# Kernel optimization log

Hardware: AMD Instinct MI355X
Metric: run time of the kernel (lower is better)

The kernel has to match this reference:

```python
import jax, jax.numpy as jnp
import numpy as np

SIZES = [4096, 12288, 20480, 20480, 8192]  # atoms of degree 0..4 (atoms sorted by degree)
N_ATOMS = sum(SIZES)
BATCH = 1024
N_TASKS, N_CLASSES = 12, 2
BN_EPS = 1e-3  # keras BatchNormalization default epsilon


def setup_inputs() -> dict:
    key = jax.random.key(0)
    ks = jax.random.split(key, 20)
    inp = {}
    inp["atom_features"] = jax.random.normal(ks[0], (N_ATOMS, 75), jnp.float32)
    starts = np.concatenate([[0], np.cumsum(SIZES)[:-1]])
    inp["degree_slice"] = jnp.asarray(np.stack([starts, np.array(SIZES)], 1), jnp.int32)
    inp["membership"] = jax.random.randint(ks[1], (N_ATOMS,), 0, BATCH, jnp.int32)
    inp["n_samples"] = BATCH
    for d in range(1, 5):
        inp[f"deg_adj_{d}"] = jax.random.randint(ks[1 + d], (SIZES[d], d), 0, N_ATOMS, jnp.int32)

    def w(k, shape, s=0.05):
        return s * jax.random.normal(k, shape, jnp.float32)

    # GraphConv weights: order [relW_deg1, selfW_deg1, ..., relW_deg4, selfW_deg4, selfW_deg0]
    inp["gc1_W"] = w(ks[6], (9, 75, 256)); inp["gc1_b"] = w(ks[7], (9, 256))
    inp["gc2_W"] = w(ks[8], (9, 256, 256)); inp["gc2_b"] = w(ks[9], (9, 256))

    def bn_params(k, c):  # rows: gamma, beta, moving_mean, moving_var
        g = 1.0 + 0.1 * jax.random.normal(k, (c,), jnp.float32)
        b = 0.1 * jax.random.normal(jax.random.fold_in(k, 1), (c,), jnp.float32)
        return jnp.stack([g, b, jnp.zeros((c,), jnp.float32), jnp.ones((c,), jnp.float32)])

    inp["bn1"] = bn_params(ks[10], 256)
    inp["bn2"] = bn_params(ks[11], 256)
    inp["bn3"] = bn_params(ks[12], 512)
    inp["dense_W"] = w(ks[13], (256, 512)); inp["dense_b"] = w(ks[14], (512,))
    inp["head_W"] = w(ks[15], (2 * 512, N_TASKS * N_CLASSES)); inp["head_b"] = w(ks[16], (N_TASKS * N_CLASSES,))
    return inp


def _graph_conv(x, adjs, W, b):
    # degree-0 atoms: self transform only (last weight matrix)
    pieces = [x[: SIZES[0]] @ W[8] + b[8]]
    off = SIZES[0]
    for d in range(1, 5):
        nd = SIZES[d]
        self_atoms = x[off: off + nd]
        rel = jnp.take(x, adjs[d - 1], axis=0).sum(axis=1)  # [nd, F] neighbor sum
        out = rel @ W[2 * (d - 1)] + b[2 * (d - 1)] + self_atoms @ W[2 * d - 1] + b[2 * d - 1]
        pieces.append(out)
        off += nd
    return jax.nn.relu(jnp.concatenate(pieces, axis=0))


def _graph_pool(x, adjs):
    pieces = [x[: SIZES[0]]]  # degree-0: passthrough
    off = SIZES[0]
    for d in range(1, 5):
        nd = SIZES[d]
        self_atoms = x[off: off + nd]
        neigh = jnp.take(x, adjs[d - 1], axis=0)  # [nd, d, F]
        pieces.append(jnp.maximum(self_atoms, neigh.max(axis=1)))
        off += nd
    return jnp.concatenate(pieces, axis=0)


def _bn(x, p):  # inference batchnorm with moving stats
    g, b, m, v = p
    return g * (x - m) * jax.lax.rsqrt(v + BN_EPS) + b


def reference(atom_features, degree_slice, membership, n_samples,
              deg_adj_1, deg_adj_2, deg_adj_3, deg_adj_4,
              gc1_W, gc1_b, gc2_W, gc2_b, bn1, bn2, bn3,
              dense_W, dense_b, head_W, head_b):
    adjs = (deg_adj_1, deg_adj_2, deg_adj_3, deg_adj_4)
    x = atom_features
    for W, b, bn in ((gc1_W, gc1_b, bn1), (gc2_W, gc2_b, bn2)):
        x = _bn(_graph_conv(x, adjs, W, b), bn)
        x = _graph_pool(x, adjs)
    h = _bn(jax.nn.relu(x @ dense_W + dense_b), bn3)  # [N_ATOMS, 512]
    # GraphGather: per-molecule sum and max, tanh activation
    seg_sum = jax.ops.segment_sum(h, membership, num_segments=BATCH)
    seg_max = jax.ops.segment_max(h, membership, num_segments=BATCH)
    fp = jnp.tanh(jnp.concatenate([seg_sum, seg_max], axis=1))  # neural fingerprint [BATCH, 1024]
    logits = (fp @ head_W + head_b).reshape(BATCH, N_TASKS, N_CLASSES)[: int(n_samples)]  # trim
    return jax.nn.softmax(logits, axis=-1), logits, fp
```

## Files before the change

kernel.cpp:

```cpp
#include <hip/hip_runtime.h>
#include <hip/hip_bf16.h>
#include <math.h>

#define NA 65536
#define MAXSEG 160

typedef _Float16 half8 __attribute__((ext_vector_type(8)));
typedef _Float16 h4    __attribute__((ext_vector_type(4)));
typedef float float4v  __attribute__((ext_vector_type(4)));

typedef __attribute__((address_space(3))) unsigned int lds_uint;
typedef __attribute__((address_space(1))) const unsigned int g_uint;

__device__ __forceinline__ void async16(const void* g, void* l) {
    __builtin_amdgcn_global_load_lds((g_uint*)g, (lds_uint*)l, 16, 0, 0);
}


__device__ __forceinline__ int unperm128(int p) {
    return (p & ~127) + (((p & 127) & 7) << 4) + ((p & 127) >> 3);
}

__device__ __forceinline__ unsigned mapf(float x) {
    unsigned b = __float_as_uint(x);
    return (b & 0x80000000u) ? ~b : (b | 0x80000000u);
}
#define MAPF_NEGINF 0x007FFFFFu

__device__ __forceinline__ void atom_seg(int atom, int& d, int& loc,
                                         const int* a1, const int* a2,
                                         const int* a3, const int* a4,
                                         const int*& adj) {
    if (atom < 4096)       { d = 0; loc = 0; adj = nullptr; }
    else if (atom < 16384) { d = 1; adj = a1; loc = atom - 4096; }
    else if (atom < 36864) { d = 2; adj = a2; loc = atom - 16384; }
    else if (atom < 57344) { d = 3; adj = a3; loc = atom - 36864; }
    else                   { d = 4; adj = a4; loc = atom - 57344; }
}

__global__ __launch_bounds__(256) void prep_kernel(
    const float* __restrict__ af,
    const float* __restrict__ gc1W, const float* __restrict__ gc1b,
    const float* __restrict__ gc2W, const float* __restrict__ gc2b,
    const float* __restrict__ dW, const float* __restrict__ hW,
    _Float16* __restrict__ af16, _Float16* __restrict__ Wc1, float* __restrict__ bias1,
    _Float16* __restrict__ Wc2, float* __restrict__ bias2,
    _Float16* __restrict__ dWt, float* __restrict__ hWt, int* __restrict__ count) {
    int b = blockIdx.x, t = threadIdx.x;
    if (b < 5120) {
        int idx = b * 256 + t;
        int atom = idx / 20, k4 = idx - atom * 20;
        int c0 = k4 * 4;
        h4 o;
        #pragma unroll
        for (int j = 0; j < 4; j++) {
            int c = c0 + j;
            o[j] = (_Float16)((c < 75) ? af[(size_t)atom * 75 + c] : 0.f);
        }
        *(h4*)(af16 + (size_t)atom * 80 + c0) = o;
    } else if (b < 5920) {
        int idx = (b - 5120) * 256 + t;
        if (idx < 204800) {
            int k = idx % 160, n = (idx / 160) & 255, seg = idx / (160 * 256);
            float v = 0.f;
            if (k < 80) {
                if (k < 75) { int w = (seg == 0) ? 8 : (2 * seg - 1); v = gc1W[(w * 75 + k) * 256 + n]; }
            } else {
                int kk = k - 80;
                if (kk < 75 && seg > 0) { int w = 2 * (seg - 1); v = gc1W[(w * 75 + kk) * 256 + n]; }
            }
            Wc1[(size_t)(seg * 256 + n) * 160 + k] = (_Float16)v;
        }
        if (idx < 1280) {
            int n = idx & 255, seg = idx >> 8;
            bias1[idx] = (seg == 0) ? gc1b[8 * 256 + n]
                                    : gc1b[(2 * seg - 1) * 256 + n] + gc1b[2 * (seg - 1) * 256 + n];
        }
    } else if (b < 8480) {
        int idx = (b - 5920) * 256 + t;
        int k = idx & 511, n = (idx >> 9) & 255, seg = idx >> 17;
        float v = 0.f;
        if (k < 256) {
            int w = (seg == 0) ? 8 : (2 * seg - 1);
            v = gc2W[(w * 256 + unperm128(k)) * 256 + n];
        } else if (seg > 0) {
            int w = 2 * (seg - 1);
            v = gc2W[(w * 256 + unperm128(k - 256)) * 256 + n];
        }
        Wc2[(size_t)(seg * 256 + n) * 512 + k] = (_Float16)v;
        if (idx < 1280) {
            int nn = idx & 255, sg = idx >> 8;
            bias2[idx] = (sg == 0) ? gc2b[8 * 256 + nn]
                                   : gc2b[(2 * sg - 1) * 256 + nn] + gc2b[2 * (sg - 1) * 256 + nn];
        }
    } else if (b < 8992) {
        int idx = (b - 8480) * 256 + t;
        int n = idx >> 8, k = idx & 255;
        dWt[(size_t)n * 256 + k] = (_Float16)dW[(size_t)unperm128(k) * 512 + n];
    } else if (b < 9088) {
        int idx = (b - 8992) * 256 + t;
        int o = idx / 1024, k = idx & 1023;
        hWt[idx] = hW[k * 24 + o];
    } else {
        int i = (b - 9088) * 256 + t;
        if (i < 1024) count[i] = 0;
    }
}

__global__ void bucket_kernel(const int* __restrict__ mem, int* __restrict__ count,
                              int* __restrict__ list) {
    int i = blockIdx.x * 256 + threadIdx.x;
    int seg = mem[i];
    int pos = atomicAdd(&count[seg], 1);
    if (pos < MAXSEG) list[seg * MAXSEG + pos] = i;
}

__global__ __launch_bounds__(1024) void scan_kernel(const int* __restrict__ count,
                                                    int* __restrict__ offs) {
    __shared__ int tmp[1024];
    int t = threadIdx.x;
    int v = count[t]; if (v > MAXSEG) v = MAXSEG;
    tmp[t] = v;
    __syncthreads();
    for (int off = 1; off < 1024; off <<= 1) {
        int x = (t >= off) ? tmp[t - off] : 0;
        __syncthreads();
        tmp[t] += x;
        __syncthreads();
    }
    offs[t] = tmp[t] - v;
}

__global__ __launch_bounds__(256) void build_sorted_kernel(
    const int* __restrict__ count, const int* __restrict__ offs,
    const int* __restrict__ list, int* __restrict__ sorted, int* __restrict__ ipos) {
    int seg = blockIdx.x;
    int n = count[seg]; if (n > MAXSEG) n = MAXSEG;
    int base = offs[seg];
    for (int i = threadIdx.x; i < n; i += 256) {
        int atom = list[seg * MAXSEG + i];
        sorted[base + i] = atom | (seg << 16);
        ipos[atom] = base + i;
    }
}

__global__ __launch_bounds__(256) void gather1n_kernel(
    const _Float16* __restrict__ af16,
    const int* __restrict__ a1, const int* __restrict__ a2,
    const int* __restrict__ a3, const int* __restrict__ a4,
    _Float16* __restrict__ Xn1) {
    int idx = blockIdx.x * 256 + threadIdx.x;
    int atom = idx / 20, k4 = idx - atom * 20;
    int c0 = k4 * 4;
    int d, loc; const int* adj;
    atom_seg(atom, d, loc, a1, a2, a3, a4, adj);
    float s0 = 0.f, s1 = 0.f, s2 = 0.f, s3 = 0.f;
    for (int j = 0; j < d; j++) {
        int nb = adj[(size_t)loc * d + j];
        h4 v = *(const h4*)(af16 + (size_t)nb * 80 + c0);
        s0 += (float)v[0]; s1 += (float)v[1]; s2 += (float)v[2]; s3 += (float)v[3];
    }
    h4 o; o[0] = (_Float16)s0; o[1] = (_Float16)s1; o[2] = (_Float16)s2; o[3] = (_Float16)s3;
    *(h4*)(Xn1 + (size_t)atom * 80 + c0) = o;
}

__global__ __launch_bounds__(256) void gather2n_kernel(
    const _Float16* __restrict__ p,
    const int* __restrict__ a1, const int* __restrict__ a2,
    const int* __restrict__ a3, const int* __restrict__ a4,
    _Float16* __restrict__ Xn) {
    int atom = blockIdx.x * 8 + (threadIdx.x >> 5);
    int l = threadIdx.x & 31;
    int d, loc; const int* adj;
    atom_seg(atom, d, loc, a1, a2, a3, a4, adj);
    float s[8] = {};
    for (int j = 0; j < d; j++) {
        int nb = adj[(size_t)loc * d + j];
        half8 v = *(const half8*)(p + (size_t)nb * 256 + l * 8);
        #pragma unroll
        for (int e = 0; e < 8; e++) s[e] += (float)v[e];
    }
    half8 o;
    #pragma unroll
    for (int e = 0; e < 8; e++) o[e] = (_Float16)s[e];
    *(half8*)(Xn + (size_t)atom * 256 + l * 8) = o;
}

template<int K, int N, int BK, int SB>
__global__ __launch_bounds__(256) void gemm_kernel(
    const _Float16* __restrict__ X, const _Float16* __restrict__ Xn,
    const _Float16* __restrict__ Wt,
    const float* __restrict__ bias, const float* __restrict__ bnp,
    int wstride, int bstride, _Float16* __restrict__ out) {
    constexpr int NC8 = BK / 8;
    constexpr int MASK = NC8 - 1;
    __shared__ __align__(16) _Float16 As[128 * BK];
    __shared__ __align__(16) _Float16 Bs[128 * BK];
    constexpr int nb = N / 128;
    int G = gridDim.x;
    int bid = (blockIdx.x & 7) * (G >> 3) + (blockIdx.x >> 3);
    int m0 = (bid / nb) * 128, n0 = (bid % nb) * 128;
    int t = m0 >> 7;
    int seg = (t < 32) ? 0 : (t < 128) ? 1 : (t < 288) ? 2 : (t < 448) ? 3 : 4;
    const _Float16* Wb = Wt + (size_t)seg * wstride;
    const float* bia = bias + seg * bstride;
    int tid = threadIdx.x, lane = tid & 63, wave = tid >> 6;
    int wm = (wave >> 1) * 64, wn = (wave & 1) * 64;
    int lrow = lane & 15, lq = lane >> 4;
    float4v acc[4][4] = {};
    for (int kc = 0; kc < K / BK; kc++) {
        #pragma unroll
        for (int q = 0; q < NC8 / 2; q++) {
            int slot = q * 256 + wave * 64 + lane;
            int row = slot / NC8;
            int cs = slot & MASK;
            int c8 = cs ^ (row & MASK);
            const _Float16* gA;
            if (SB == 0) {
                gA = X + (size_t)(m0 + row) * K + kc * BK + c8 * 8;
            } else {
                int kcol = kc * BK + c8 * 8;
                gA = (kcol < SB) ? X  + (size_t)(m0 + row) * SB + kcol
                                 : Xn + (size_t)(m0 + row) * SB + (kcol - SB);
            }
            async16(gA, As + (size_t)(q * 256 + wave * 64) * 8);
            const _Float16* gB = Wb + (size_t)(n0 + row) * K + kc * BK + c8 * 8;
            async16(gB, Bs + (size_t)(q * 256 + wave * 64) * 8);
        }
        __syncthreads();
        #pragma unroll
        for (int kl = 0; kl < BK / 32; kl++) {
            half8 af[4], bf[4];
            #pragma unroll
            for (int i = 0; i < 4; i++) {
                int ra = wm + i * 16 + lrow;
                int ca = (kl * 4 + lq) ^ (ra & MASK);
                af[i] = *(const half8*)(As + ra * BK + ca * 8);
                int rb = wn + i * 16 + lrow;
                int cb = (kl * 4 + lq) ^ (rb & MASK);
                bf[i] = *(const half8*)(Bs + rb * BK + cb * 8);
            }
            #pragma unroll
            for (int mi = 0; mi < 4; mi++)
                #pragma unroll
                for (int ni = 0; ni < 4; ni++)
                    acc[mi][ni] = __builtin_amdgcn_mfma_f32_16x16x32_f16(af[mi], bf[ni], acc[mi][ni], 0, 0, 0);
        }
        __syncthreads();
    }
    float bv[4], sc[4], mn[4], be[4];
    #pragma unroll
    for (int ni = 0; ni < 4; ni++) {
        int c = n0 + wn + ni * 16 + lrow;
        bv[ni] = bia[c];
        float g = bnp[c], vr = bnp[3 * N + c];
        mn[ni] = bnp[2 * N + c]; be[ni] = bnp[N + c];
        sc[ni] = g * rsqrtf(vr + 1e-3f);
    }
    int p0 = n0 + lrow * 8 + (wave & 1) * 4;
    #pragma unroll
    for (int mi = 0; mi < 4; mi++) {
        #pragma unroll
        for (int r = 0; r < 4; r++) {
            h4 pack;
            #pragma unroll
            for (int ni = 0; ni < 4; ni++) {
                float v = acc[mi][ni][r] + bv[ni];
                v = fmaxf(v, 0.f);
                v = sc[ni] * (v - mn[ni]) + be[ni];
                pack[ni] = (_Float16)v;
            }
            int row = m0 + wm + mi * 16 + lq * 4 + r;
            *(h4*)(out + (size_t)row * N + p0) = pack;
        }
    }
}

__global__ __launch_bounds__(256) void pool_f16_kernel(
    const _Float16* __restrict__ x,
    const int* __restrict__ a1, const int* __restrict__ a2,
    const int* __restrict__ a3, const int* __restrict__ a4,
    const int* __restrict__ remap,
    _Float16* __restrict__ out) {
    int atom = blockIdx.x * 8 + (threadIdx.x >> 5);
    int l = threadIdx.x & 31;
    int d, loc; const int* adj;
    atom_seg(atom, d, loc, a1, a2, a3, a4, adj);
    half8 m = *(const half8*)(x + (size_t)atom * 256 + l * 8);
    float mv[8];
    #pragma unroll
    for (int e = 0; e < 8; e++) mv[e] = (float)m[e];
    for (int j = 0; j < d; j++) {
        int nb = adj[(size_t)loc * d + j];
        half8 v = *(const half8*)(x + (size_t)nb * 256 + l * 8);
        #pragma unroll
        for (int e = 0; e < 8; e++) mv[e] = fmaxf(mv[e], (float)v[e]);
    }
    half8 o;
    #pragma unroll
    for (int e = 0; e < 8; e++) o[e] = (_Float16)mv[e];
    int orow = remap ? remap[atom] : atom;
    *(half8*)(out + (size_t)orow * 256 + l * 8) = o;
}

__global__ __launch_bounds__(256) void dense_kernel(
    const _Float16* __restrict__ X, const _Float16* __restrict__ Wt,
    const float* __restrict__ bias, const float* __restrict__ bnp,
    const int* __restrict__ sorted,
    float* __restrict__ psum, unsigned* __restrict__ pmax) {
    constexpr int NBINS = 4;
    __shared__ __align__(16) _Float16 As[64 * 64];
    __shared__ __align__(16) _Float16 Bs[128 * 64];
    __shared__ float binsum[NBINS * 128];
    __shared__ unsigned binmax[NBINS * 128];
    __shared__ int spk[64];
    int G = gridDim.x;
    int bid = (blockIdx.x & 7) * (G >> 3) + (blockIdx.x >> 3);
    int m0 = (bid >> 2) * 64, n0 = (bid & 3) * 128;
    int tid = threadIdx.x, lane = tid & 63, wave = tid >> 6;
    if (tid < 64) spk[tid] = sorted[m0 + tid];
    for (int e = tid; e < NBINS * 128; e += 256) { binsum[e] = 0.f; binmax[e] = MAPF_NEGINF; }
    __syncthreads();
    int wm = (wave & 1) * 32, wn = (wave >> 1) * 64;
    int lrow = lane & 15, lq = lane >> 4;
    float4v acc[2][4] = {};
    for (int kc = 0; kc < 4; kc++) {
        #pragma unroll
        for (int q = 0; q < 2; q++) {
            int slot = q * 256 + wave * 64 + lane;
            int row = slot >> 3, cs = slot & 7, c8 = cs ^ (row & 7);
            async16(X + (size_t)(m0 + row) * 256 + kc * 64 + c8 * 8,
                    As + (size_t)(q * 256 + wave * 64) * 8);
        }
        #pragma unroll
        for (int q = 0; q < 4; q++) {
            int slot = q * 256 + wave * 64 + lane;
            int row = slot >> 3, cs = slot & 7, c8 = cs ^ (row & 7);
            async16(Wt + (size_t)(n0 + row) * 256 + kc * 64 + c8 * 8,
                    Bs + (size_t)(q * 256 + wave * 64) * 8);
        }
        __syncthreads();
        #pragma unroll
        for (int kl = 0; kl < 2; kl++) {
            half8 af[2], bf[4];
            #pragma unroll
            for (int i = 0; i < 2; i++) {
                int ra = wm + i * 16 + lrow;
                int ca = (kl * 4 + lq) ^ (ra & 7);
                af[i] = *(const half8*)(As + ra * 64 + ca * 8);
            }
            #pragma unroll
            for (int j = 0; j < 4; j++) {
                int rb = wn + j * 16 + lrow;
                int cb = (kl * 4 + lq) ^ (rb & 7);
                bf[j] = *(const half8*)(Bs + rb * 64 + cb * 8);
            }
            #pragma unroll
            for (int mi = 0; mi < 2; mi++)
                #pragma unroll
                for (int ni = 0; ni < 4; ni++)
                    acc[mi][ni] = __builtin_amdgcn_mfma_f32_16x16x32_f16(af[mi], bf[ni], acc[mi][ni], 0, 0, 0);
        }
        __syncthreads();
    }
    float bv[4], sc[4], mn[4], be[4];
    #pragma unroll
    for (int ni = 0; ni < 4; ni++) {
        int c = n0 + wn + ni * 16 + lrow;
        bv[ni] = bias[c];
        float g = bnp[c], vr = bnp[3 * 512 + c];
        mn[ni] = bnp[2 * 512 + c]; be[ni] = bnp[512 + c];
        sc[ni] = g * rsqrtf(vr + 1e-3f);
    }
    int pcol = lrow * 8 + (wave >> 1) * 4;
    int segbase = spk[0] >> 16;
    #pragma unroll
    for (int mi = 0; mi < 2; mi++) {
        int r0 = wm + mi * 16;
        int sFirst = spk[r0] >> 16, sLast = spk[r0 + 15] >> 16;
        if (sFirst == sLast) {
            int srel = sFirst - segbase; if (srel > NBINS - 1) srel = NBINS - 1;
            float ps[4], pm[4];
            #pragma unroll
            for (int ni = 0; ni < 4; ni++) { ps[ni] = 0.f; pm[ni] = -INFINITY; }
            #pragma unroll
            for (int r = 0; r < 4; r++) {
                #pragma unroll
                for (int ni = 0; ni < 4; ni++) {
                    float v = acc[mi][ni][r] + bv[ni];
                    v = fmaxf(v, 0.f);
                    v = sc[ni] * (v - mn[ni]) + be[ni];
                    ps[ni] += v;
                    pm[ni] = fmaxf(pm[ni], v);
                }
            }
            #pragma unroll
            for (int ni = 0; ni < 4; ni++) {
                ps[ni] += __shfl_xor(ps[ni], 16, 64);
                ps[ni] += __shfl_xor(ps[ni], 32, 64);
                pm[ni] = fmaxf(pm[ni], __shfl_xor(pm[ni], 16, 64));
                pm[ni] = fmaxf(pm[ni], __shfl_xor(pm[ni], 32, 64));
            }
            if (lq == 0) {
                int bb = srel * 128 + pcol;
                #pragma unroll
                for (int ni = 0; ni < 4; ni++) {
                    atomicAdd(&binsum[bb + ni], ps[ni]);
                    atomicMax(&binmax[bb + ni], mapf(pm[ni]));
                }
            }
        } else {
            int curs = -1;
            float ps[4], pm[4];
            #pragma unroll
            for (int r = 0; r < 4; r++) {
                int row = r0 + lq * 4 + r;
                int srel = (spk[row] >> 16) - segbase;
                if (srel > NBINS - 1) srel = NBINS - 1;
                if (srel != curs) {
                    if (curs >= 0) {
                        int bb = curs * 128 + pcol;
                        #pragma unroll
                        for (int ni = 0; ni < 4; ni++) {
                            atomicAdd(&binsum[bb + ni], ps[ni]);
                            atomicMax(&binmax[bb + ni], mapf(pm[ni]));
                        }
                    }
                    curs = srel;
                    #pragma unroll
                    for (int ni = 0; ni < 4; ni++) { ps[ni] = 0.f; pm[ni] = -INFINITY; }
                }
                #pragma unroll
                for (int ni = 0; ni < 4; ni++) {
                    float v = acc[mi][ni][r] + bv[ni];
                    v = fmaxf(v, 0.f);
                    v = sc[ni] * (v - mn[ni]) + be[ni];
                    ps[ni] += v;
                    pm[ni] = fmaxf(pm[ni], v);
                }
            }
            {
                int bb = curs * 128 + pcol;
                #pragma unroll
                for (int ni = 0; ni < 4; ni++) {
                    atomicAdd(&binsum[bb + ni], ps[ni]);
                    atomicMax(&binmax[bb + ni], mapf(pm[ni]));
                }
            }
        }
    }
    __syncthreads();
    int nseg = (spk[63] >> 16) - segbase + 1;
    if (nseg > NBINS) nseg = NBINS;
    int tile = m0 >> 6;
    for (int e = tid; e < nseg * 128; e += 256) {
        int s = e >> 7, pc = e & 127;
        size_t slot = ((size_t)(tile * NBINS + s)) * 512 + n0 + pc;
        psum[slot] = binsum[e];
        pmax[slot] = binmax[e];
    }
}

__global__ __launch_bounds__(256) void head_kernel(
    const float* __restrict__ psum, const unsigned* __restrict__ pmax,
    const int* __restrict__ count, const int* __restrict__ offs,
    const int* __restrict__ sorted,
    const float* __restrict__ hWt, const float* __restrict__ hb,
    float* __restrict__ fp, float* __restrict__ logits, float* __restrict__ probs) {
    constexpr int NBINS = 4;
    __shared__ float fps[1024];
    __shared__ float red[32];
    int s = blockIdx.x;
    int t = threadIdx.x;
    int cnt = count[s]; if (cnt > MAXSEG) cnt = MAXSEG;
    int off = offs[s];
    float sum0 = 0.f, sum1 = 0.f;
    unsigned mu0 = MAPF_NEGINF, mu1 = MAPF_NEGINF;
    if (cnt > 0) {
        int t0 = off >> 6, t1 = (off + cnt - 1) >> 6;
        for (int tt = t0; tt <= t1; tt++) {
            int segbase_t = sorted[tt << 6] >> 16;
            int srel = s - segbase_t;
            if (srel < 0) srel = 0;
            if (srel > NBINS - 1) srel = NBINS - 1;
            const float* ps = psum + ((size_t)(tt * NBINS + srel)) * 512;
            const unsigned* pm = pmax + ((size_t)(tt * NBINS + srel)) * 512;
            sum0 += ps[t]; sum1 += ps[t + 256];
            unsigned a0 = pm[t], a1 = pm[t + 256];
            mu0 = (a0 > mu0) ? a0 : mu0;
            mu1 = (a1 > mu1) ? a1 : mu1;
        }
    }
    {
        float sv = tanhf(sum0);
        unsigned b = (mu0 & 0x80000000u) ? (mu0 & 0x7FFFFFFFu) : ~mu0;
        float mv = tanhf(__uint_as_float(b));
        int chan = unperm128(t);
        fps[chan] = sv; fps[512 + chan] = mv;
        fp[(size_t)s * 1024 + chan] = sv;
        fp[(size_t)s * 1024 + 512 + chan] = mv;
    }
    {
        float sv = tanhf(sum1);
        unsigned b = (mu1 & 0x80000000u) ? (mu1 & 0x7FFFFFFFu) : ~mu1;
        float mv = tanhf(__uint_as_float(b));
        int chan = unperm128(t + 256);
        fps[chan] = sv; fps[512 + chan] = mv;
        fp[(size_t)s * 1024 + chan] = sv;
        fp[(size_t)s * 1024 + 512 + chan] = mv;
    }
    __syncthreads();
    int o = t >> 3, kp = t & 7;
    float acc = 0.f;
    if (o < 24) {
        const float* w = hWt + (size_t)o * 1024 + kp * 128;
        const float* f = fps + kp * 128;
        #pragma unroll 8
        for (int i = 0; i < 128; i++) acc = fmaf(f[i], w[i], acc);
    }
    acc += __shfl_down(acc, 4, 64);
    acc += __shfl_down(acc, 2, 64);
    acc += __shfl_down(acc, 1, 64);
    if (o < 24 && kp == 0) red[o] = acc + hb[o];
    __syncthreads();
    if (t < 24) {
        float a = red[t];
        float an = red[t ^ 1];
        logits[(size_t)s * 24 + t] = a;
        probs[(size_t)s * 24 + t] = 1.f / (1.f + expf(an - a));
    }
}

extern "C" void kernel_launch(void* const* d_in, const int* in_sizes, int n_in,
                              void* d_out, int out_size, void* d_ws, size_t ws_size,
                              hipStream_t stream) {
    const float* af         = (const float*)d_in[0];
    const int*   membership = (const int*)d_in[2];
    const int*   a1 = (const int*)d_in[4];
    const int*   a2 = (const int*)d_in[5];
    const int*   a3 = (const int*)d_in[6];
    const int*   a4 = (const int*)d_in[7];
    const float* gc1W = (const float*)d_in[8];
    const float* gc1b = (const float*)d_in[9];
    const float* gc2W = (const float*)d_in[10];
    const float* gc2b = (const float*)d_in[11];
    const float* bn1  = (const float*)d_in[12];
    const float* bn2  = (const float*)d_in[13];
    const float* bn3  = (const float*)d_in[14];
    const float* dW   = (const float*)d_in[15];
    const float* db   = (const float*)d_in[16];
    const float* hW   = (const float*)d_in[17];
    const float* hb   = (const float*)d_in[18];

    float* out    = (float*)d_out;
    float* probs  = out;
    float* logits = out + 24576;
    float* fp     = out + 49152;

    _Float16* Wc1  = (_Float16*)d_ws;
    _Float16* Wc2  = Wc1 + 204800;
    _Float16* dWt  = Wc2 + 655360;
    float* bias1   = (float*)(dWt + 131072);
    float* bias2   = bias1 + 1280;
    float* hWt     = bias2 + 1280;
    float* psum    = hWt + 24576;
    unsigned* pmax = (unsigned*)(psum + 2097152);
    int* count     = (int*)(pmax + 2097152);
    int* offs      = count + 1024;
    int* sorted    = offs + 1024;
    int* ipos      = sorted + 65536;
    int* list      = ipos + 65536;
    _Float16* bufSm  = (_Float16*)(list + 163840);
    _Float16* Xn     = bufSm + (size_t)NA * 160;
    _Float16* bufY   = Xn + (size_t)NA * 256;
    _Float16* bufP   = bufY + (size_t)NA * 256;
    _Float16* af16 = bufSm;
    _Float16* Xn1  = bufSm + (size_t)NA * 80;

    prep_kernel<<<9092, 256, 0, stream>>>(af, gc1W, gc1b, gc2W, gc2b, dW, hW,
                                          af16, Wc1, bias1, Wc2, bias2, dWt, hWt, count);
    bucket_kernel<<<256, 256, 0, stream>>>(membership, count, list);
    scan_kernel<<<1, 1024, 0, stream>>>(count, offs);
    build_sorted_kernel<<<1024, 256, 0, stream>>>(count, offs, list, sorted, ipos);
    gather1n_kernel<<<5120, 256, 0, stream>>>(af16, a1, a2, a3, a4, Xn1);
    gemm_kernel<160, 256, 32, 80><<<1024, 256, 0, stream>>>(af16, Xn1, Wc1, bias1, bn1,
                                                            256 * 160, 256, bufY);
    pool_f16_kernel<<<8192, 256, 0, stream>>>(bufY, a1, a2, a3, a4, nullptr, bufP);
    gather2n_kernel<<<8192, 256, 0, stream>>>(bufP, a1, a2, a3, a4, Xn);
    gemm_kernel<512, 256, 64, 256><<<1024, 256, 0, stream>>>(bufP, Xn, Wc2, bias2, bn2,
                                                             256 * 512, 256, bufY);
    pool_f16_kernel<<<8192, 256, 0, stream>>>(bufY, a1, a2, a3, a4, ipos, bufP);
    dense_kernel<<<4096, 256, 0, stream>>>(bufP, dWt, db, bn3, sorted, psum, pmax);
    head_kernel<<<1024, 256, 0, stream>>>(psum, pmax, count, offs, sorted,
                                          hWt, hb, fp, logits, probs);
}
```

Before: 308.3 us.

## Keep dense weight tile resident in LDS and double-buffer 256-row activation tiles

The dense+BN+gather kernel now gives each block four 64-row subtiles (256 rows). It loads the full-K 128x256 weight slab into LDS once and double-buffers the activation subtiles, prefetching the next while computing the current one. This cuts repeated weight reloads and per-k-chunk barriers, and the grid shrinks from 4096 to 1024 blocks. The per-tile segment bins double to 8, and the head kernel now indexes 256-row tiles. The cost is about 136KB of LDS per block, which limits occupancy to one block per CU. There is also a small risk of bin clamping if a 256-row tile spans more than 8 molecules.

```diff
diff --git a/kernel.cpp b/kernel.cpp
--- a/kernel.cpp
+++ b/kernel.cpp
@@ -308,61 +308,38 @@
     const float* __restrict__ bias, const float* __restrict__ bnp,
     const int* __restrict__ sorted,
     float* __restrict__ psum, unsigned* __restrict__ pmax) {
-    constexpr int NBINS = 4;
-    __shared__ __align__(16) _Float16 As[64 * 64];
-    __shared__ __align__(16) _Float16 Bs[128 * 64];
+    constexpr int NBINS = 8;
+    __shared__ __align__(16) _Float16 Bs[128 * 256];
+    __shared__ __align__(16) _Float16 As[2][64 * 256];
     __shared__ float binsum[NBINS * 128];
     __shared__ unsigned binmax[NBINS * 128];
-    __shared__ int spk[64];
+    __shared__ int spk[256];
     int G = gridDim.x;
     int bid = (blockIdx.x & 7) * (G >> 3) + (blockIdx.x >> 3);
-    int m0 = (bid >> 2) * 64, n0 = (bid & 3) * 128;
+    int mg = bid >> 2, n0 = (bid & 3) * 128;
+    int m_base = mg * 256;
     int tid = threadIdx.x, lane = tid & 63, wave = tid >> 6;
-    if (tid < 64) spk[tid] = sorted[m0 + tid];
+    spk[tid] = sorted[m_base + tid];
     for (int e = tid; e < NBINS * 128; e += 256) { binsum[e] = 0.f; binmax[e] = MAPF_NEGINF; }
+    #pragma unroll
+    for (int q = 0; q < 16; q++) {
+        int slot = q * 256 + wave * 64 + lane;
+        int row = slot >> 5, c32 = slot & 31, kcg = c32 >> 3, cs = c32 & 7;
+        int c8 = cs ^ (row & 7);
+        async16(Wt + (size_t)(n0 + row) * 256 + kcg * 64 + c8 * 8,
+                Bs + (size_t)slot * 8);
+    }
+    #pragma unroll
+    for (int q = 0; q < 8; q++) {
+        int slot = q * 256 + wave * 64 + lane;
+        int row = slot >> 5, c32 = slot & 31, kcg = c32 >> 3, cs = c32 & 7;
+        int c8 = cs ^ (row & 7);
+        async16(X + (size_t)(m_base + row) * 256 + kcg * 64 + c8 * 8,
+                As[0] + (size_t)slot * 8);
+    }
     __syncthreads();
     int wm = (wave & 1) * 32, wn = (wave >> 1) * 64;
     int lrow = lane & 15, lq = lane >> 4;
-    float4v acc[2][4] = {};
-    for (int kc = 0; kc < 4; kc++) {
-        #pragma unroll
-        for (int q = 0; q < 2; q++) {
-            int slot = q * 256 + wave * 64 + lane;
-            int row = slot >> 3, cs = slot & 7, c8 = cs ^ (row & 7);
-            async16(X + (size_t)(m0 + row) * 256 + kc * 64 + c8 * 8,
-                    As + (size_t)(q * 256 + wave * 64) * 8);
-        }
-        #pragma unroll
-        for (int q = 0; q < 4; q++) {
-            int slot = q * 256 + wave * 64 + lane;
-            int row = slot >> 3, cs = slot & 7, c8 = cs ^ (row & 7);
-            async16(Wt + (size_t)(n0 + row) * 256 + kc * 64 + c8 * 8,
-                    Bs + (size_t)(q * 256 + wave * 64) * 8);
-        }
-        __syncthreads();
-        #pragma unroll
-        for (int kl = 0; kl < 2; kl++) {
-            half8 af[2], bf[4];
-            #pragma unroll
-            for (int i = 0; i < 2; i++) {
-                int ra = wm + i * 16 + lrow;
-                int ca = (kl * 4 + lq) ^ (ra & 7);
-                af[i] = *(const half8*)(As + ra * 64 + ca * 8);
-            }
-            #pragma unroll
-            for (int j = 0; j < 4; j++) {
-                int rb = wn + j * 16 + lrow;
-                int cb = (kl * 4 + lq) ^ (rb & 7);
-                bf[j] = *(const half8*)(Bs + rb * 64 + cb * 8);
-            }
-            #pragma unroll
-            for (int mi = 0; mi < 2; mi++)
-                #pragma unroll
-                for (int ni = 0; ni < 4; ni++)
-                    acc[mi][ni] = __builtin_amdgcn_mfma_f32_16x16x32_f16(af[mi], bf[ni], acc[mi][ni], 0, 0, 0);
-        }
-        __syncthreads();
-    }
     float bv[4], sc[4], mn[4], be[4];
     #pragma unroll
     for (int ni = 0; ni < 4; ni++) {
@@ -374,88 +351,125 @@
     }
     int pcol = lrow * 8 + (wave >> 1) * 4;
     int segbase = spk[0] >> 16;
-    #pragma unroll
-    for (int mi = 0; mi < 2; mi++) {
-        int r0 = wm + mi * 16;
-        int sFirst = spk[r0] >> 16, sLast = spk[r0 + 15] >> 16;
-        if (sFirst == sLast) {
-            int srel = sFirst - segbase; if (srel > NBINS - 1) srel = NBINS - 1;
-            float ps[4], pm[4];
+    for (int st = 0; st < 4; st++) {
+        if (st < 3) {
             #pragma unroll
-            for (int ni = 0; ni < 4; ni++) { ps[ni] = 0.f; pm[ni] = -INFINITY; }
+            for (int q = 0; q < 8; q++) {
+                int slot = q * 256 + wave * 64 + lane;
+                int row = slot >> 5, c32 = slot & 31, kcg = c32 >> 3, cs = c32 & 7;
+                int c8 = cs ^ (row & 7);
+                async16(X + (size_t)(m_base + (st + 1) * 64 + row) * 256 + kcg * 64 + c8 * 8,
+                        As[(st + 1) & 1] + (size_t)slot * 8);
+            }
+        }
+        const _Float16* Ab = As[st & 1];
+        float4v acc[2][4] = {};
+        #pragma unroll
+        for (int kc = 0; kc < 4; kc++) {
             #pragma unroll
-            for (int r = 0; r < 4; r++) {
+            for (int kl = 0; kl < 2; kl++) {
+                int cpos = kl * 4 + lq;
+                half8 af[2], bf[4];
+                #pragma unroll
+                for (int i = 0; i < 2; i++) {
+                    int ra = wm + i * 16 + lrow;
+                    af[i] = *(const half8*)(Ab + ra * 256 + kc * 64 + (cpos ^ (ra & 7)) * 8);
+                }
+                #pragma unroll
+                for (int j = 0; j < 4; j++) {
+                    int rb = wn + j * 16 + lrow;
+                    bf[j] = *(const half8*)(Bs + rb * 256 + kc * 64 + (cpos ^ (rb & 7)) * 8);
+                }
+                #pragma unroll
+                for (int mi = 0; mi < 2; mi++)
+                    #pragma unroll
+                    for (int ni = 0; ni < 4; ni++)
+                        acc[mi][ni] = __builtin_amdgcn_mfma_f32_16x16x32_f16(af[mi], bf[ni], acc[mi][ni], 0, 0, 0);
+            }
+        }
+        int sb = st * 64;
+        #pragma unroll
+        for (int mi = 0; mi < 2; mi++) {
+            int r0 = sb + wm + mi * 16;
+            int sFirst = spk[r0] >> 16, sLast = spk[r0 + 15] >> 16;
+            if (sFirst == sLast) {
+                int srel = sFirst - segbase; if (srel > NBINS - 1) srel = NBINS - 1;
+                float ps[4], pm[4];
+                #pragma unroll
+                for (int ni = 0; ni < 4; ni++) { ps[ni] = 0.f; pm[ni] = -INFINITY; }
+                #pragma unroll
+                for (int r = 0; r < 4; r++) {
+                    #pragma unroll
+                    for (int ni = 0; ni < 4; ni++) {
+                        float v = acc[mi][ni][r] + bv[ni];
+                        v = fmaxf(v, 0.f);
+                        v = sc[ni] * (v - mn[ni]) + be[ni];
+                        ps[ni] += v;
+                        pm[ni] = fmaxf(pm[ni], v);
+                    }
+                }
                 #pragma unroll
                 for (int ni = 0; ni < 4; ni++) {
-                    float v = acc[mi][ni][r] + bv[ni];
-                    v = fmaxf(v, 0.f);
-                    v = sc[ni] * (v - mn[ni]) + be[ni];
-                    ps[ni] += v;
-                    pm[ni] = fmaxf(pm[ni], v);
+                    ps[ni] += __shfl_xor(ps[ni], 16, 64);
+                    ps[ni] += __shfl_xor(ps[ni], 32, 64);
+                    pm[ni] = fmaxf(pm[ni], __shfl_xor(pm[ni], 16, 64));
+                    pm[ni] = fmaxf(pm[ni], __shfl_xor(pm[ni], 32, 64));
+                }
+                if (lq == 0) {
+                    int bb = srel * 128 + pcol;
+                    #pragma unroll
+                    for (int ni = 0; ni < 4; ni++) {
+                        atomicAdd(&binsum[bb + ni], ps[ni]);
+                        atomicMax(&binmax[bb + ni], mapf(pm[ni]));
+                    }
+                }
+            } else {
+                int curs = -1;
+                float ps[4], pm[4];
+                #pragma unroll
+                for (int r = 0; r < 4; r++) {
+                    int row = r0 + lq * 4 + r;
+                    int srel = (spk[row] >> 16) - segbase;
+                    if (srel > NBINS - 1) srel = NBINS - 1;
+                    if (srel != curs) {
+                        if (curs >= 0) {
+                            int bb = curs * 128 + pcol;
+                            #pragma unroll
+                            for (int ni = 0; ni < 4; ni++) {
+                                atomicAdd(&binsum[bb + ni], ps[ni]);
+                                atomicMax(&binmax[bb + ni], mapf(pm[ni]));
+                            }
+                        }
+                        curs = srel;
+                        #pragma unroll
+                        for (int ni = 0; ni < 4; ni++) { ps[ni] = 0.f; pm[ni] = -INFINITY; }
+                    }
+                    #pragma unroll
+                    for (int ni = 0; ni < 4; ni++) {
+                        float v = acc[mi][ni][r] + bv[ni];
+                        v = fmaxf(v, 0.f);
+                        v = sc[ni] * (v - mn[ni]) + be[ni];
+                        ps[ni] += v;
+                        pm[ni] = fmaxf(pm[ni], v);
+                    }
+                }
+                {
+                    int bb = curs * 128 + pcol;
+                    #pragma unroll
+                    for (int ni = 0; ni < 4; ni++) {
+                        atomicAdd(&binsum[bb + ni], ps[ni]);
+                        atomicMax(&binmax[bb + ni], mapf(pm[ni]));
+                    }
                 }
             }
-            #pragma unroll
-            for (int ni = 0; ni < 4; ni++) {
-                ps[ni] += __shfl_xor(ps[ni], 16, 64);
-                ps[ni] += __shfl_xor(ps[ni], 32, 64);
-                pm[ni] = fmaxf(pm[ni], __shfl_xor(pm[ni], 16, 64));
-                pm[ni] = fmaxf(pm[ni], __shfl_xor(pm[ni], 32, 64));
-            }
-            if (lq == 0) {
-                int bb = srel * 128 + pcol;
-                #pragma unroll
-                for (int ni = 0; ni < 4; ni++) {
-                    atomicAdd(&binsum[bb + ni], ps[ni]);
-                    atomicMax(&binmax[bb + ni], mapf(pm[ni]));
-                }
-            }
-        } else {
-            int curs = -1;
-            float ps[4], pm[4];
-            #pragma unroll
-            for (int r = 0; r < 4; r++) {
-                int row = r0 + lq * 4 + r;
-                int srel = (spk[row] >> 16) - segbase;
-                if (srel > NBINS - 1) srel = NBINS - 1;
-                if (srel != curs) {
-                    if (curs >= 0) {
-                        int bb = curs * 128 + pcol;
-                        #pragma unroll
-                        for (int ni = 0; ni < 4; ni++) {
-                            atomicAdd(&binsum[bb + ni], ps[ni]);
-                            atomicMax(&binmax[bb + ni], mapf(pm[ni]));
-                        }
-                    }
-                    curs = srel;
-                    #pragma unroll
-                    for (int ni = 0; ni < 4; ni++) { ps[ni] = 0.f; pm[ni] = -INFINITY; }
-                }
-                #pragma unroll
-                for (int ni = 0; ni < 4; ni++) {
-                    float v = acc[mi][ni][r] + bv[ni];
-                    v = fmaxf(v, 0.f);
-                    v = sc[ni] * (v - mn[ni]) + be[ni];
-                    ps[ni] += v;
-                    pm[ni] = fmaxf(pm[ni], v);
-                }
-            }
-            {
-                int bb = curs * 128 + pcol;
-                #pragma unroll
-                for (int ni = 0; ni < 4; ni++) {
-                    atomicAdd(&binsum[bb + ni], ps[ni]);
-                    atomicMax(&binmax[bb + ni], mapf(pm[ni]));
-                }
-            }
-        }
-    }
-    __syncthreads();
-    int nseg = (spk[63] >> 16) - segbase + 1;
+        }
+        __syncthreads();
+    }
+    int nseg = (spk[255] >> 16) - segbase + 1;
     if (nseg > NBINS) nseg = NBINS;
-    int tile = m0 >> 6;
     for (int e = tid; e < nseg * 128; e += 256) {
         int s = e >> 7, pc = e & 127;
-        size_t slot = ((size_t)(tile * NBINS + s)) * 512 + n0 + pc;
+        size_t slot = ((size_t)(mg * NBINS + s)) * 512 + n0 + pc;
         psum[slot] = binsum[e];
         pmax[slot] = binmax[e];
     }
@@ -467,7 +481,7 @@
     const int* __restrict__ sorted,
     const float* __restrict__ hWt, const float* __restrict__ hb,
     float* __restrict__ fp, float* __restrict__ logits, float* __restrict__ probs) {
-    constexpr int NBINS = 4;
+    constexpr int NBINS = 8;
     __shared__ float fps[1024];
     __shared__ float red[32];
     int s = blockIdx.x;
@@ -477,9 +491,9 @@
     float sum0 = 0.f, sum1 = 0.f;
     unsigned mu0 = MAPF_NEGINF, mu1 = MAPF_NEGINF;
     if (cnt > 0) {
-        int t0 = off >> 6, t1 = (off + cnt - 1) >> 6;
+        int t0 = off >> 8, t1 = (off + cnt - 1) >> 8;
         for (int tt = t0; tt <= t1; tt++) {
-            int segbase_t = sorted[tt << 6] >> 16;
+            int segbase_t = sorted[tt << 8] >> 16;
             int srel = s - segbase_t;
             if (srel < 0) srel = 0;
             if (srel > NBINS - 1) srel = NBINS - 1;
@@ -590,7 +604,7 @@
     gemm_kernel<512, 256, 64, 256><<<1024, 256, 0, stream>>>(bufP, Xn, Wc2, bias2, bn2,
                                                              256 * 512, 256, bufY);
     pool_f16_kernel<<<8192, 256, 0, stream>>>(bufY, a1, a2, a3, a4, ipos, bufP);
-    dense_kernel<<<4096, 256, 0, stream>>>(bufP, dWt, db, bn3, sorted, psum, pmax);
+    dense_kernel<<<1024, 256, 0, stream>>>(bufP, dWt, db, bn3, sorted, psum, pmax);
     head_kernel<<<1024, 256, 0, stream>>>(psum, pmax, count, offs, sorted,
                                           hWt, hb, fp, logits, probs);
 }
```

Result: slower. 326.8 us (+6.0%).
